# Kernel tuning notes

Measured on AMD Instinct MI355X. Metric: run time of the kernel, lower is better.

The kernel has to match this reference:

```python
import jax, jax.numpy as jnp
import numpy as np

B, S, D, H, HD = 2, 2048, 2048, 16, 128  # batch, seq, embed, heads, head_dim


def setup_inputs() -> dict:
    key = jax.random.key(0)
    k0, k1, k2 = jax.random.split(key, 3)
    hidden_states = jax.random.normal(k0, (B, S, D), dtype=jnp.float32)
    # fused QKV projection: [D, H*HD + 2*HD] (multi-query: single shared K and V head)
    W_attn = jax.random.normal(k1, (D, H * HD + 2 * HD), dtype=jnp.float32) * 0.02
    b_attn = jnp.zeros((H * HD + 2 * HD,), dtype=jnp.float32)
    W_proj = jax.random.normal(k2, (D, D), dtype=jnp.float32) * 0.02
    b_proj = jnp.zeros((D,), dtype=jnp.float32)
    # causal mask, broadcastable to (B, Q, H, K); True = attend
    attention_mask = jnp.tril(jnp.ones((S, S), dtype=bool))[None, :, None, :]
    return {
        "hidden_states": hidden_states,
        "W_attn": W_attn,
        "b_attn": b_attn,
        "W_proj": W_proj,
        "b_proj": b_proj,
        "attention_mask": attention_mask,
    }


def reference(hidden_states, W_attn, b_attn, W_proj, b_proj, attention_mask):
    # fused QKV, then split into Q (H heads) and shared K/V (multi-query)
    qkv = hidden_states @ W_attn + b_attn          # (B, S, H*HD + 2*HD)
    q = qkv[..., : H * HD].reshape(B, S, H, HD)    # (B, Q, H, hd)
    key_t = qkv[..., H * HD : H * HD + HD]         # (B, K, hd) shared K head
    value = qkv[..., H * HD + HD :]                # (B, K, hd) shared V head

    # dtype == softmax_dtype (fp32) -> upcast=False, unscale=1
    scale_factor = 1.0 / (HD ** 0.5)               # scale_attn_weights
    attn_weights = jnp.einsum("bqhd,bkd->bqhk", q, key_t) * scale_factor
    mask_value = jnp.finfo(jnp.float32).min
    attn_weights = jnp.where(attention_mask, attn_weights, mask_value)
    attn_weights = jax.nn.softmax(attn_weights, axis=-1)

    attn_output = jnp.einsum("bqhk,bkd->bqhd", attn_weights, value)
    attn_output = attn_output.reshape(B, S, H * HD)
    return attn_output @ W_proj + b_proj           # (B, S, D)
```

## Files before the change

### kernel.cpp

```cpp
#include <hip/hip_runtime.h>
#include <math.h>

constexpr int cB  = 2;
constexpr int cS  = 2048;
constexpr int cD  = 2048;
constexpr int cH  = 16;
constexpr int cHD = 128;
constexpr int cNQKV = cH * cHD + 2 * cHD;

typedef __attribute__((ext_vector_type(8))) short bf16x8;
typedef __attribute__((ext_vector_type(4))) float f32x4;
typedef __attribute__((ext_vector_type(16))) float f32x16;

__device__ __forceinline__ short f2bf(float f) {
    union { float f; unsigned u; } v; v.f = f;
    unsigned r = (v.u + 0x7FFFu + ((v.u >> 16) & 1u)) >> 16;
    return (short)r;
}

__device__ __forceinline__ unsigned pk_bf16(float lo, float hi_) {
    return (unsigned)(unsigned short)f2bf(lo)
         | ((unsigned)(unsigned short)f2bf(hi_) << 16);
}

typedef __attribute__((address_space(3))) void lds_t;
typedef const __attribute__((address_space(1))) void gbl_t;
__device__ __forceinline__ void gld16(const void* g, void* l) {
    __builtin_amdgcn_global_load_lds((gbl_t*)g, (lds_t*)l, 16, 0, 0);
}

__global__ __launch_bounds__(256) void conv_bf16(
    const float* __restrict__ src, short* __restrict__ dst)
{
    size_t i = ((size_t)blockIdx.x * 256 + threadIdx.x) * 8;
    float4 a = *(const float4*)(src + i);
    float4 b = *(const float4*)(src + i + 4);
    bf16x8 o;
    o[0] = f2bf(a.x); o[1] = f2bf(a.y); o[2] = f2bf(a.z); o[3] = f2bf(a.w);
    o[4] = f2bf(b.x); o[5] = f2bf(b.y); o[6] = f2bf(b.z); o[7] = f2bf(b.w);
    *(bf16x8*)(dst + i) = o;
}

__global__ __launch_bounds__(256) void transpose_bf16(
    const float* __restrict__ src, short* __restrict__ dst, int K, int N)
{
    __shared__ short t[32][33];
    const int n0 = blockIdx.x * 32, k0 = blockIdx.y * 32;
    const int x = threadIdx.x & 31, y = threadIdx.x >> 5;
#pragma unroll
    for (int i = 0; i < 4; ++i)
        t[y + 8 * i][x] = f2bf(src[(size_t)(k0 + y + 8 * i) * N + n0 + x]);
    __syncthreads();
#pragma unroll
    for (int i = 0; i < 4; ++i)
        dst[(size_t)(n0 + y + 8 * i) * K + k0 + x] = t[x][y + 8 * i];
}

template<bool BF16_OUT>
__global__ __launch_bounds__(256) void gemm_mfma(
    const short* __restrict__ A, const short* __restrict__ Bt,
    const float* __restrict__ bias, void* __restrict__ Cout,
    int M, int N, int K, float qscale, int qcols)
{
    __shared__ short As[128 * 32];
    __shared__ short Bs[128 * 32];

    const int tid = threadIdx.x;
    const int lane = tid & 63, n16 = lane & 15, quad = lane >> 4;
    const int wave = tid >> 6, wm = wave >> 1, wn = wave & 1;
    const int m0 = blockIdx.y * 128, n0 = blockIdx.x * 128;

    f32x4 acc[4][4];
#pragma unroll
    for (int i = 0; i < 4; ++i)
#pragma unroll
        for (int j = 0; j < 4; ++j) acc[i][j] = 0.0f;

    const int s0 = tid, s1 = tid + 256;
    const short* Ag0 = A  + (size_t)(m0 + (s0 >> 2)) * K + (s0 & 3) * 8;
    const short* Ag1 = A  + (size_t)(m0 + (s1 >> 2)) * K + (s1 & 3) * 8;
    const short* Bg0 = Bt + (size_t)(n0 + (s0 >> 2)) * K + (s0 & 3) * 8;
    const short* Bg1 = Bt + (size_t)(n0 + (s1 >> 2)) * K + (s1 & 3) * 8;

    for (int k0 = 0; k0 < K; k0 += 32) {
        gld16(Ag0 + k0, &As[s0 * 8]);
        gld16(Ag1 + k0, &As[s1 * 8]);
        gld16(Bg0 + k0, &Bs[s0 * 8]);
        gld16(Bg1 + k0, &Bs[s1 * 8]);
        __syncthreads();
        bf16x8 af[4], bfr[4];
#pragma unroll
        for (int mt = 0; mt < 4; ++mt)
            af[mt] = *(const bf16x8*)&As[(wm * 64 + mt * 16 + n16) * 32 + quad * 8];
#pragma unroll
        for (int nt = 0; nt < 4; ++nt)
            bfr[nt] = *(const bf16x8*)&Bs[(wn * 64 + nt * 16 + n16) * 32 + quad * 8];
#pragma unroll
        for (int mt = 0; mt < 4; ++mt)
#pragma unroll
            for (int nt = 0; nt < 4; ++nt)
                acc[mt][nt] = __builtin_amdgcn_mfma_f32_16x16x32_bf16(
                    af[mt], bfr[nt], acc[mt][nt], 0, 0, 0);
        __syncthreads();
    }

#pragma unroll
    for (int nt = 0; nt < 4; ++nt) {
        const int col = n0 + wn * 64 + nt * 16 + n16;
        const float bv = bias[col];
        const float sc = (col < qcols) ? qscale : 1.0f;
#pragma unroll
        for (int mt = 0; mt < 4; ++mt)
#pragma unroll
            for (int r = 0; r < 4; ++r) {
                const int row = m0 + wm * 64 + mt * 16 + quad * 4 + r;
                const float v = (acc[mt][nt][r] + bv) * sc;
                if (BF16_OUT) ((short*)Cout)[(size_t)row * N + col] = f2bf(v);
                else          ((float*)Cout)[(size_t)row * N + col] = v;
            }
    }
}

__global__ __launch_bounds__(256) void prep_v(
    const short* __restrict__ qkvb, short* __restrict__ Vt)
{
    const int b  = blockIdx.y;
    const int k0 = blockIdx.x * 64;
    const int t  = threadIdx.x;
#pragma unroll
    for (int i = 0; i < 32; ++i) {
        int idx = i * 256 + t;
        int hd = idx >> 6, key = idx & 63;
        Vt[((size_t)b * cHD + hd) * cS + k0 + key] =
            qkvb[((size_t)(b * cS + k0 + key)) * cNQKV + cH * cHD + cHD + hd];
    }
}

__global__ __launch_bounds__(256, 2) void attn_mfma(
    const short* __restrict__ qkvb, const short* __restrict__ Vt,
    short* __restrict__ out)
{
    const int tid  = threadIdx.x;
    const int wave = tid >> 6;
    const int lane = tid & 63;
    const int q32  = lane & 31;
    const int hi   = lane >> 5;
    const int qhalf = wave & 1;
    const int khalf = wave >> 1;
    const int h  = blockIdx.y;
    const int b  = blockIdx.z;

    __shared__ __align__(16) float Obuf[2][32][128];
    __shared__ float Lbuf[2][32];
    __shared__ float Linv[2][32];

    const short* kglob = qkvb + (size_t)b * cS * cNQKV + cH * cHD;
    const short* vbase = Vt + (size_t)b * cHD * cS;

#pragma unroll 1
    for (int seg = 0; seg < 2; ++seg) {
        const int qt = seg ? (int)blockIdx.x : 31 - (int)blockIdx.x;
        const int qb = qt * 64;
        const int qg = qb + qhalf * 32 + q32;
        const int nkt = qt + 1;

        bf16x8 qf[8];
        {
            const short* qbase = qkvb + ((size_t)(b * cS) + qg) * cNQKV
                               + h * cHD + hi * 8;
#pragma unroll
            for (int dblk = 0; dblk < 8; ++dblk)
                qf[dblk] = *(const bf16x8*)(qbase + dblk * 16);
        }

        f32x16 oc[4];
#pragma unroll
        for (int i = 0; i < 4; ++i) oc[i] = 0.0f;
        float lp = 0.0f;

        const short* krbase = kglob + (size_t)(khalf * 32 + q32) * cNQKV + hi * 8;

        bf16x8 kfc[8];
#pragma unroll
        for (int dblk = 0; dblk < 8; ++dblk)
            kfc[dblk] = *(const bf16x8*)(krbase + dblk * 16);

#pragma unroll 1
        for (int kt = 0; kt < nkt; ++kt) {
            const int k0 = kt * 64;

            f32x16 sc = 0.0f;
            __builtin_amdgcn_s_setprio(1);
#pragma unroll
            for (int dblk = 0; dblk < 8; ++dblk)
                sc = __builtin_amdgcn_mfma_f32_32x32x16_bf16(
                    kfc[dblk], qf[dblk], sc, 0, 0, 0);
            __builtin_amdgcn_s_setprio(0);

            if (kt + 1 < nkt) {
                const short* krn = krbase + (size_t)(k0 + 64) * cNQKV;
#pragma unroll
                for (int dblk = 0; dblk < 8; ++dblk)
                    kfc[dblk] = *(const bf16x8*)(krn + dblk * 16);
            }

            const bool diag = (kt == nkt - 1);
            float e[16];
#pragma unroll
            for (int r = 0; r < 16; ++r) {
                float s = sc[r];
                if (diag) {
                    int kgl = k0 + khalf * 32 + (r & 3) + 8 * (r >> 2) + 4 * hi;
                    if (kgl > qg) s = -1e30f;
                }
                float p = __expf(s);
                lp += p;
                e[r] = p;
            }

            bf16x8 vf0[4], vf1[4];
#pragma unroll
            for (int dtile = 0; dtile < 4; ++dtile) {
                const short* vr = vbase + (size_t)(dtile * 32 + q32) * cS
                                + k0 + khalf * 32 + hi * 8;
                vf0[dtile] = *(const bf16x8*)(vr);
                vf1[dtile] = *(const bf16x8*)(vr + 16);
            }

            bf16x8 pa[2];
#pragma unroll
            for (int kblk = 0; kblk < 2; ++kblk) {
                const int rb = 8 * kblk;
                unsigned wA0 = pk_bf16(e[rb + 0], e[rb + 1]);
                unsigned wA1 = pk_bf16(e[rb + 2], e[rb + 3]);
                unsigned wB0 = pk_bf16(e[rb + 4], e[rb + 5]);
                unsigned wB1 = pk_bf16(e[rb + 6], e[rb + 7]);
                unsigned keep0 = hi ? wB0 : wA0, keep1 = hi ? wB1 : wA1;
                unsigned send0 = hi ? wA0 : wB0, send1 = hi ? wA1 : wB1;
                unsigned recv0 = (unsigned)__shfl_xor((int)send0, 32);
                unsigned recv1 = (unsigned)__shfl_xor((int)send1, 32);
                union { unsigned u[4]; bf16x8 v; } uu;
                uu.u[0] = hi ? recv0 : keep0;
                uu.u[1] = hi ? recv1 : keep1;
                uu.u[2] = hi ? keep0 : recv0;
                uu.u[3] = hi ? keep1 : recv1;
                pa[kblk] = uu.v;
            }

            __builtin_amdgcn_s_setprio(1);
#pragma unroll
            for (int dtile = 0; dtile < 4; ++dtile) {
                oc[dtile] = __builtin_amdgcn_mfma_f32_32x32x16_bf16(
                    pa[0], vf0[dtile], oc[dtile], 0, 0, 0);
                oc[dtile] = __builtin_amdgcn_mfma_f32_32x32x16_bf16(
                    pa[1], vf1[dtile], oc[dtile], 0, 0, 0);
            }
            __builtin_amdgcn_s_setprio(0);
        }

        lp += __shfl_xor(lp, 32);
        __syncthreads();
        if (khalf == 1) {
            float* ob = &Obuf[qhalf][0][0];
#pragma unroll
            for (int dtile = 0; dtile < 4; ++dtile)
#pragma unroll
                for (int r = 0; r < 16; ++r) {
                    const int q = (r & 3) + 8 * (r >> 2) + 4 * hi;
                    ob[q * 128 + dtile * 32 + q32] = oc[dtile][r];
                }
            if (hi == 0) Lbuf[qhalf][q32] = lp;
        }
        __syncthreads();
        if (khalf == 0) {
            const float* ob = &Obuf[qhalf][0][0];
#pragma unroll
            for (int dtile = 0; dtile < 4; ++dtile)
#pragma unroll
                for (int r = 0; r < 16; ++r) {
                    const int q = (r & 3) + 8 * (r >> 2) + 4 * hi;
                    oc[dtile][r] += ob[q * 128 + dtile * 32 + q32];
                }
            lp += Lbuf[qhalf][q32];
            if (hi == 0) Linv[qhalf][q32] = 1.0f / lp;
        }
        __syncthreads();
        if (khalf == 0) {
            f32x4 invv[4];
#pragma unroll
            for (int g = 0; g < 4; ++g)
                invv[g] = *(const f32x4*)&Linv[qhalf][g * 8 + hi * 4];
            short* obase = out + ((size_t)(b * cS) + qb + qhalf * 32) * cD + h * cHD;
#pragma unroll
            for (int dtile = 0; dtile < 4; ++dtile)
#pragma unroll
                for (int r = 0; r < 16; ++r) {
                    const int q = (r & 3) + 8 * (r >> 2) + 4 * hi;
                    obase[(size_t)q * cD + dtile * 32 + q32] =
                        f2bf(oc[dtile][r] * invv[r >> 2][r & 3]);
                }
        }
    }
}

extern "C" void kernel_launch(void* const* d_in, const int* in_sizes, int n_in,
                              void* d_out, int out_size, void* d_ws, size_t ws_size,
                              hipStream_t stream)
{
    const float* hidden = (const float*)d_in[0];
    const float* W_attn = (const float*)d_in[1];
    const float* b_attn = (const float*)d_in[2];
    const float* W_proj = (const float*)d_in[3];
    const float* b_proj = (const float*)d_in[4];
    float* out = (float*)d_out;

    const int M = cB * cS;
    short* qkvb = (short*)d_ws;
    short* Ah   = qkvb + (size_t)M * cNQKV;
    short* Wb   = Ah   + (size_t)M * cD;
    short* Wpb  = Wb   + (size_t)cNQKV * cD;
    short* Vt   = Wpb  + (size_t)cD * cD;
    short* attno = Ah;

    const float scale = 0.088388347648318447f;

    conv_bf16<<<(size_t)M * cD / 2048, 256, 0, stream>>>(hidden, Ah);
    transpose_bf16<<<dim3(cNQKV / 32, cD / 32), 256, 0, stream>>>(W_attn, Wb, cD, cNQKV);
    transpose_bf16<<<dim3(cD / 32, cD / 32), 256, 0, stream>>>(W_proj, Wpb, cD, cD);

    gemm_mfma<true><<<dim3(cNQKV / 128, M / 128), 256, 0, stream>>>(
        Ah, Wb, b_attn, qkvb, M, cNQKV, cD, scale, cH * cHD);

    prep_v<<<dim3(cS / 64, cB), 256, 0, stream>>>(qkvb, Vt);

    attn_mfma<<<dim3(16, cH, cB), 256, 0, stream>>>(qkvb, Vt, attno);

    gemm_mfma<false><<<dim3(cD / 128, M / 128), 256, 0, stream>>>(
        attno, Wpb, b_proj, out, M, cD, cD, 1.0f, 0);
}
```

Before: 385.8 us.

## Pre-swizzle K/V into MFMA fragment layout and prefetch V tiles

Adds a prep kernel that rearranges the shared K and V heads into a fragment-major layout, so each lane does fully coalesced, contiguous 16-byte loads matching the MFMA operand order. The attention kernel then reads K and V from these buffers and prefetches the next V tile after the PV MFMAs, so global loads overlap with compute instead of stalling inside the loop. In exchange it adds an extra kernel launch, extra workspace and more live vector registers.

New measurement: 347.9 us. -9.8%, faster.

```diff
diff --git a/kernel.cpp b/kernel.cpp
--- a/kernel.cpp
+++ b/kernel.cpp
@@ -136,9 +136,38 @@
     }
 }
 
+__global__ __launch_bounds__(256) void prep_kvf(
+    const short* __restrict__ qkvb, const short* __restrict__ Vt,
+    short* __restrict__ Kf, short* __restrict__ Vf)
+{
+    const int gidx = blockIdx.x * 256 + threadIdx.x;
+    if (gidx < 65536) {
+        const int idx = gidx;
+        const int r32  = idx & 31;
+        const int hi   = (idx >> 5) & 1;
+        const int dblk = (idx >> 6) & 7;
+        const int g    = (idx >> 9) & 63;
+        const int b    = idx >> 15;
+        const short* src = qkvb + ((size_t)(b * cS) + g * 32 + r32) * cNQKV
+                         + cH * cHD + dblk * 16 + hi * 8;
+        *(bf16x8*)(Kf + (size_t)idx * 8) = *(const bf16x8*)src;
+    } else {
+        const int idx = gidx - 65536;
+        const int l     = idx & 63;
+        const int dtile = (idx >> 6) & 3;
+        const int kblk  = (idx >> 8) & 1;
+        const int kt2   = (idx >> 9) & 63;
+        const int b     = idx >> 15;
+        const int q32 = l & 31, hi = l >> 5;
+        const short* src = Vt + ((size_t)(b * cHD) + dtile * 32 + q32) * cS
+                         + kt2 * 32 + kblk * 16 + hi * 8;
+        *(bf16x8*)(Vf + (size_t)idx * 8) = *(const bf16x8*)src;
+    }
+}
+
 __global__ __launch_bounds__(256, 2) void attn_mfma(
-    const short* __restrict__ qkvb, const short* __restrict__ Vt,
-    short* __restrict__ out)
+    const short* __restrict__ qkvb, const short* __restrict__ Kf,
+    const short* __restrict__ Vf, short* __restrict__ out)
 {
     const int tid  = threadIdx.x;
     const int wave = tid >> 6;
@@ -154,9 +183,6 @@
     __shared__ float Lbuf[2][32];
     __shared__ float Linv[2][32];
 
-    const short* kglob = qkvb + (size_t)b * cS * cNQKV + cH * cHD;
-    const short* vbase = Vt + (size_t)b * cHD * cS;
-
 #pragma unroll 1
     for (int seg = 0; seg < 2; ++seg) {
         const int qt = seg ? (int)blockIdx.x : 31 - (int)blockIdx.x;
@@ -178,12 +204,17 @@
         for (int i = 0; i < 4; ++i) oc[i] = 0.0f;
         float lp = 0.0f;
 
-        const short* krbase = kglob + (size_t)(khalf * 32 + q32) * cNQKV + hi * 8;
-
-        bf16x8 kfc[8];
+        const short* kfp = Kf + ((size_t)(b * 64) + khalf) * 4096
+                         + hi * 256 + q32 * 8;
+        const short* vfp = Vf + ((size_t)(b * 64) + khalf) * 4096 + lane * 8;
+
+        bf16x8 kfc[8], vfc[8];
 #pragma unroll
         for (int dblk = 0; dblk < 8; ++dblk)
-            kfc[dblk] = *(const bf16x8*)(krbase + dblk * 16);
+            kfc[dblk] = *(const bf16x8*)(kfp + dblk * 512);
+#pragma unroll
+        for (int u = 0; u < 8; ++u)
+            vfc[u] = *(const bf16x8*)(vfp + u * 512);
 
 #pragma unroll 1
         for (int kt = 0; kt < nkt; ++kt) {
@@ -198,10 +229,10 @@
             __builtin_amdgcn_s_setprio(0);
 
             if (kt + 1 < nkt) {
-                const short* krn = krbase + (size_t)(k0 + 64) * cNQKV;
+                const short* kn = kfp + (size_t)(kt + 1) * 8192;
 #pragma unroll
                 for (int dblk = 0; dblk < 8; ++dblk)
-                    kfc[dblk] = *(const bf16x8*)(krn + dblk * 16);
+                    kfc[dblk] = *(const bf16x8*)(kn + dblk * 512);
             }
 
             const bool diag = (kt == nkt - 1);
@@ -216,15 +247,6 @@
                 float p = __expf(s);
                 lp += p;
                 e[r] = p;
-            }
-
-            bf16x8 vf0[4], vf1[4];
-#pragma unroll
-            for (int dtile = 0; dtile < 4; ++dtile) {
-                const short* vr = vbase + (size_t)(dtile * 32 + q32) * cS
-                                + k0 + khalf * 32 + hi * 8;
-                vf0[dtile] = *(const bf16x8*)(vr);
-                vf1[dtile] = *(const bf16x8*)(vr + 16);
             }
 
             bf16x8 pa[2];
@@ -251,11 +273,18 @@
 #pragma unroll
             for (int dtile = 0; dtile < 4; ++dtile) {
                 oc[dtile] = __builtin_amdgcn_mfma_f32_32x32x16_bf16(
-                    pa[0], vf0[dtile], oc[dtile], 0, 0, 0);
+                    pa[0], vfc[dtile], oc[dtile], 0, 0, 0);
                 oc[dtile] = __builtin_amdgcn_mfma_f32_32x32x16_bf16(
-                    pa[1], vf1[dtile], oc[dtile], 0, 0, 0);
+                    pa[1], vfc[4 + dtile], oc[dtile], 0, 0, 0);
             }
             __builtin_amdgcn_s_setprio(0);
+
+            if (kt + 1 < nkt) {
+                const short* vn = vfp + (size_t)(kt + 1) * 8192;
+#pragma unroll
+                for (int u = 0; u < 8; ++u)
+                    vfc[u] = *(const bf16x8*)(vn + u * 512);
+            }
         }
 
         lp += __shfl_xor(lp, 32);
@@ -320,6 +349,8 @@
     short* Wb   = Ah   + (size_t)M * cD;
     short* Wpb  = Wb   + (size_t)cNQKV * cD;
     short* Vt   = Wpb  + (size_t)cD * cD;
+    short* Kf   = Vt   + (size_t)cB * cHD * cS;
+    short* Vf   = Kf   + (size_t)cB * cS * cHD;
     short* attno = Ah;
 
     const float scale = 0.088388347648318447f;
@@ -332,8 +363,9 @@
         Ah, Wb, b_attn, qkvb, M, cNQKV, cD, scale, cH * cHD);
 
     prep_v<<<dim3(cS / 64, cB), 256, 0, stream>>>(qkvb, Vt);
-
-    attn_mfma<<<dim3(16, cH, cB), 256, 0, stream>>>(qkvb, Vt, attno);
+    prep_kvf<<<512, 256, 0, stream>>>(qkvb, Vt, Kf, Vf);
+
+    attn_mfma<<<dim3(16, cH, cB), 256, 0, stream>>>(qkvb, Kf, Vf, attno);
 
     gemm_mfma<false><<<dim3(cD / 128, M / 128), 256, 0, stream>>>(
         attno, Wpb, b_proj, out, M, cD, cD, 1.0f, 0);
```
